# Kernel tuning notes

Measured on AMD Instinct MI355X. Metric: run time of the kernel, lower is better.

Reference implementation:

```python
import jax, jax.numpy as jnp
import numpy as np

B, T, D = 4, 8192, 512
H, BS = 8, 16


def setup_inputs() -> dict:
    key = jax.random.key(0)
    ks = jax.random.split(key, 7)
    s = 1.0 / np.sqrt(D)
    return {
        "x": jax.random.normal(ks[0], (B, T, D), dtype=jnp.float32),
        "Wq": jax.random.normal(ks[1], (D, D), dtype=jnp.float32) * s,
        "bq": jax.random.normal(ks[2], (D,), dtype=jnp.float32) * 0.02,
        "Wk": jax.random.normal(ks[3], (D, D), dtype=jnp.float32) * s,
        "bk": jax.random.normal(ks[4], (D,), dtype=jnp.float32) * 0.02,
        "Wv": jax.random.normal(ks[5], (D, D), dtype=jnp.float32) * s,
        "bv": jax.random.normal(ks[6], (D,), dtype=jnp.float32) * 0.02,
    }


def reference(x, Wq, bq, Wk, bk, Wv, bv):
    b, t, d_model = x.shape
    nb = t // BS          # number of blocks
    dh = d_model // H     # per-head dim
    # [B,T,D] -> [B,nb,BS,D] -> [B,BS,nb,D]: attention runs across blocks
    xb = x.reshape(b, nb, BS, d_model).transpose(0, 2, 1, 3)
    # projections (torch Linear: x @ W.T + b)
    q = xb @ Wq.T + bq
    k = xb @ Wk.T + bk
    v = xb @ Wv.T + bv
    # split heads: [B,BS,nb,H,dh] -> [B,BS,H,nb,dh]
    q = q.reshape(b, BS, nb, H, dh).transpose(0, 1, 3, 2, 4)
    k = k.reshape(b, BS, nb, H, dh).transpose(0, 1, 3, 2, 4)
    v = v.reshape(b, BS, nb, H, dh).transpose(0, 1, 3, 2, 4)
    scale = d_model ** (-0.5)  # note: full dim, as in the original
    attn = jnp.einsum('bshnd,bshmd->bshnm', q, k) * scale  # [B,BS,H,nb,nb]
    attn = jax.nn.softmax(attn, axis=-1)
    out = jnp.einsum('bshnm,bshmd->bshnd', attn, v)        # [B,BS,H,nb,dh]
    # merge heads and undo block permute
    out = out.transpose(0, 1, 3, 2, 4).reshape(b, BS, nb, d_model)
    out = out.transpose(0, 2, 1, 3).reshape(b, t, d_model)
    return out
```

## Files before the change

### kernel.cpp

```cpp
#include <hip/hip_runtime.h>
#include <hip/hip_bf16.h>
#include <cstdint>
#include <cstddef>

#define Bsz 4
#define Tsz 8192
#define Dsz 512
#define Hn 8
#define BSn 16
#define NBn 512
#define DHn 64
#define NQKV 1536
#define MROWS 32768

#define SCL 0.06375870136f
#define ATT_M 8.0f

typedef __attribute__((ext_vector_type(8))) short short8;
typedef __attribute__((ext_vector_type(4))) float float4f;

__device__ __forceinline__ uint16_t f2b(float f) {
  union { float f; uint32_t u; } v; v.f = f;
  uint32_t u = v.u;
  return (uint16_t)((u + 0x7fffu + ((u >> 16) & 1u)) >> 16);
}

__device__ __forceinline__ uint32_t pk2(float a, float b) {
  union { float f; uint32_t u; } x, y; x.f = a; y.f = b;
  return __builtin_amdgcn_perm(y.u + 0x8000u, x.u + 0x8000u, 0x07060302u);
}

__device__ __forceinline__ uint32_t pk2t(float a, float b) {
  union { float f; uint32_t u; } x, y; x.f = a; y.f = b;
  return __builtin_amdgcn_perm(y.u, x.u, 0x07060302u);
}

__device__ __forceinline__ void gl_lds16(const void* g, void* l) {
  __builtin_amdgcn_global_load_lds(
      (const __attribute__((address_space(1))) unsigned int*)g,
      (__attribute__((address_space(3))) unsigned int*)l, 16, 0, 0);
}

#define XBLK (MROWS * Dsz / 1024)
__global__ void cvt_kernel(const float* __restrict__ x, const float* __restrict__ Wq,
                           const float* __restrict__ Wk, const float* __restrict__ Wv,
                           uint16_t* __restrict__ xb, uint16_t* __restrict__ wc) {
  int bid = blockIdx.x;
  if (bid < XBLK) {
    int i = (bid * 256 + threadIdx.x) * 4;
    float4 v = *(const float4*)(x + i);
    uint64_t o = (uint64_t)pk2(v.x, v.y) | ((uint64_t)pk2(v.z, v.w) << 32);
    *(uint64_t*)(xb + i) = o;
  } else {
    int i = ((bid - XBLK) * 256 + threadIdx.x) * 4;
    int row = i >> 9;
    int col = i & 511;
    const float* src = (row < 512) ? Wq : ((row < 1024) ? Wk : Wv);
    float4 v = *(const float4*)(src + (size_t)(row & 511) * 512 + col);
    uint64_t o = (uint64_t)pk2(v.x, v.y) | ((uint64_t)pk2(v.z, v.w) << 32);
    *(uint64_t*)(wc + i) = o;
  }
}

#define BM 128
#define BN 128
#define BK 64

__global__ __launch_bounds__(256, 4) void gemm_qkv(
    const uint16_t* __restrict__ Xb, const uint16_t* __restrict__ Wc,
    const float* __restrict__ bq, const float* __restrict__ bkp,
    const float* __restrict__ bv, uint16_t* __restrict__ Qp,
    uint16_t* __restrict__ Kp, uint16_t* __restrict__ Vtmp) {
  __shared__ uint16_t As[BM * BK];
  __shared__ uint16_t Bs[BN * BK];
  const int tid = threadIdx.x;
  const int wave = tid >> 6, lane = tid & 63;
  const int lrow = lane & 15, quad = lane >> 4;

  int g = blockIdx.x;
  int xcd = g & 7, ii = g >> 3;
  int mt = xcd * 32 + ii / 12;
  int nt = ii - (ii / 12) * 12;
  const int m0 = mt * BM;
  const int n0 = nt * BN;
  const int wm = (wave >> 1) * 64, wn = (wave & 1) * 64;

  float4f acc[4][4] = {};

  for (int k0 = 0; k0 < Dsz; k0 += BK) {
    __syncthreads();
#pragma unroll
    for (int p = 0; p < 4; ++p) {
      int cbase = p * 256 + wave * 64;
      int c = cbase + lane;
      int row = c >> 3, pos = c & 7;
      int kc = (pos ^ (row & 7)) * 8;
      gl_lds16(Xb + (size_t)(m0 + row) * Dsz + k0 + kc, As + cbase * 8);
    }
#pragma unroll
    for (int p = 0; p < 4; ++p) {
      int cbase = p * 256 + wave * 64;
      int c = cbase + lane;
      int row = c >> 3, pos = c & 7;
      int kc = (pos ^ (row & 7)) * 8;
      gl_lds16(Wc + (size_t)(n0 + row) * Dsz + k0 + kc, Bs + cbase * 8);
    }
    __syncthreads();

#pragma unroll
    for (int h = 0; h < 2; ++h) {
      short8 af[4], bf[4];
#pragma unroll
      for (int i = 0; i < 4; ++i) {
        int rowA = wm + i * 16 + lrow;
        af[i] = *(const short8*)(As + rowA * BK + (((h * 4 + quad) ^ (rowA & 7)) * 8));
      }
#pragma unroll
      for (int j = 0; j < 4; ++j) {
        int rowB = wn + j * 16 + lrow;
        bf[j] = *(const short8*)(Bs + rowB * BK + (((h * 4 + quad) ^ (rowB & 7)) * 8));
      }
#pragma unroll
      for (int i = 0; i < 4; ++i)
#pragma unroll
        for (int j = 0; j < 4; ++j)
          acc[i][j] = __builtin_amdgcn_mfma_f32_16x16x32_bf16(af[i], bf[j], acc[i][j], 0, 0, 0);
    }
  }

  const int region = n0 >> 9;
  const float* bias = (region == 0) ? bq : ((region == 1) ? bkp : bv);
  const float mult = (region == 0) ? SCL : 1.0f;
  const int bb = m0 >> 13;
  const int nbbase = ((m0 & 8191) >> 4) + (wm >> 4);
  const int nv0 = (n0 & 511) + wn;

  if (region < 2) {
    uint16_t* dst = (region == 0) ? Qp : Kp;
#pragma unroll
    for (int j = 0; j < 4; ++j) {
      int nl = nv0 + j * 16 + lrow;
      int hh = nl >> 6, dh = nl & 63;
      float bval = bias[nl];
      size_t base = (size_t)bb * 4194304 + (size_t)hh * 32768 +
                    (size_t)nbbase * 64 + dh + (size_t)(quad * 4) * 262144;
#pragma unroll
      for (int i = 0; i < 4; ++i)
#pragma unroll
        for (int r = 0; r < 4; ++r)
          dst[base + (size_t)r * 262144 + (size_t)i * 64] =
              f2b((acc[i][j][r] + bval) * mult);
    }
  } else {
#pragma unroll
    for (int j = 0; j < 4; ++j) {
      int nl = nv0 + j * 16 + lrow;
      float bval = bias[nl];
#pragma unroll
      for (int i = 0; i < 4; ++i) {
        int tok = m0 + wm + i * 16 + quad * 4;
#pragma unroll
        for (int r = 0; r < 4; ++r)
          Vtmp[(size_t)(tok + r) * 512 + nl] = f2b(acc[i][j][r] + bval);
      }
    }
  }
}

__global__ __launch_bounds__(256) void vtrans(const uint16_t* __restrict__ Vtmp,
                                              uint16_t* __restrict__ Vt) {
  __shared__ uint16_t tile[64 * 64];
  int bx = blockIdx.x;
  const int nt = bx & 7; bx >>= 3;
  const int h = bx & 7; bx >>= 3;
  const int s = bx & 15;
  const int b = bx >> 4;
  const int tid = threadIdx.x;

  {
    int i = tid >> 2;
    int token = b * Tsz + (nt * 64 + i) * BSn + s;
    const uint16_t* src = Vtmp + (size_t)token * 512 + h * 64;
#pragma unroll
    for (int hh = 0; hh < 2; ++hh) {
      int ch = (tid & 3) * 2 + hh;
      short8 v = *(const short8*)(src + ch * 8);
      int pc = ch ^ (i & 7);
      *(short8*)(tile + i * 64 + pc * 8) = v;
    }
  }
  __syncthreads();
  {
    int dh = tid & 63, seg = tid >> 6;
    short8 v1, v2;
#pragma unroll
    for (int k = 0; k < 8; ++k) {
      int nb_l = seg * 16 + k;
      v1[k] = (short)tile[nb_l * 64 + (((dh >> 3) ^ (nb_l & 7)) * 8) + (dh & 7)];
    }
#pragma unroll
    for (int k = 0; k < 8; ++k) {
      int nb_l = seg * 16 + 8 + k;
      v2[k] = (short)tile[nb_l * 64 + (((dh >> 3) ^ (nb_l & 7)) * 8) + (dh & 7)];
    }
    size_t obase = ((((size_t)b * 16 + s) * 8 + h) * 64 + dh) * 512 + nt * 64 + seg * 16;
    *(short8*)(Vt + obase) = v1;
    *(short8*)(Vt + obase + 8) = v2;
  }
}

__global__ __launch_bounds__(256, 3) void attn_kernel(
    const uint16_t* __restrict__ Qp, const uint16_t* __restrict__ Kp,
    const uint16_t* __restrict__ Vt, float* __restrict__ out) {
  __shared__ uint16_t Ks[2][32 * 64];
  __shared__ uint16_t Vs[2][64 * 32];
  __shared__ uint16_t Ps[4][4][16 * 32];

  int bx = blockIdx.x;
  const int qh = bx & 1; bx >>= 1;
  const int h = bx & 7; bx >>= 3;
  const int s = bx & 15;
  const int b = bx >> 4;

  const int tid = threadIdx.x;
  const int w = tid >> 6, lane = tid & 63;
  const int lrow = lane & 15, quad = lane >> 4;

  const size_t sh = (((size_t)b * 16 + s) * 8 + h);
  const uint16_t* Qb = Qp + (sh << 15);
  const uint16_t* Kb = Kp + (sh << 15);
  const uint16_t* Vb = Vt + (sh << 15);

  short8 qB[4][2];
  const int q0 = qh * 256 + w * 64;
#pragma unroll
  for (int qs = 0; qs < 4; ++qs) {
    const uint16_t* qp = Qb + (size_t)(q0 + qs * 16 + lrow) * 64;
    qB[qs][0] = *(const short8*)(qp + quad * 8);
    qB[qs][1] = *(const short8*)(qp + 32 + quad * 8);
  }

  float4f O[4][4] = {};
  float l_acc[4] = {0.f, 0.f, 0.f, 0.f};

  const int kr = w * 8 + (lane >> 3);
  const int kcs = (lane & 7) ^ (kr & 7);
  const int vr = w * 16 + (lane >> 2);
  const int vcs = (lane & 3) ^ ((vr >> 1) & 3);

  const int sw = (lrow >> 1) & 3;
  const float4f negm = {-ATT_M, -ATT_M, -ATT_M, -ATT_M};

#define ATT_STAGE(buf, kv0_) do {                                             \
    gl_lds16(Kb + (size_t)((kv0_) + kr) * 64 + kcs * 8, &Ks[buf][w * 512]);   \
    gl_lds16(Vb + (size_t)vr * 512 + (kv0_) + vcs * 8, &Vs[buf][w * 512]);    \
  } while (0)

  ATT_STAGE(0, 0);
  __syncthreads();

  for (int it = 0; it < 16; ++it) {
    const int cur = it & 1;
    if (it < 15) ATT_STAGE(cur ^ 1, (it + 1) * 32);

    {
      short8 kA[2][2];
#pragma unroll
      for (int kt = 0; kt < 2; ++kt) {
        int row = kt * 16 + lrow;
#pragma unroll
        for (int kc = 0; kc < 2; ++kc) {
          int cc = (kc * 4 + quad) ^ (row & 7);
          kA[kt][kc] = *(const short8*)(&Ks[cur][row * 64 + cc * 8]);
        }
      }
#pragma unroll
      for (int qs = 0; qs < 4; ++qs) {
        float4f c0 = negm, c1 = negm;
        __builtin_amdgcn_s_setprio(1);
        c0 = __builtin_amdgcn_mfma_f32_16x16x32_bf16(kA[0][0], qB[qs][0], c0, 0, 0, 0);
        c0 = __builtin_amdgcn_mfma_f32_16x16x32_bf16(kA[0][1], qB[qs][1], c0, 0, 0, 0);
        c1 = __builtin_amdgcn_mfma_f32_16x16x32_bf16(kA[1][0], qB[qs][0], c1, 0, 0, 0);
        c1 = __builtin_amdgcn_mfma_f32_16x16x32_bf16(kA[1][1], qB[qs][1], c1, 0, 0, 0);
        __builtin_amdgcn_s_setprio(0);

        float p00 = __builtin_amdgcn_exp2f(c0[0]);
        float p01 = __builtin_amdgcn_exp2f(c0[1]);
        float p02 = __builtin_amdgcn_exp2f(c0[2]);
        float p03 = __builtin_amdgcn_exp2f(c0[3]);
        float p10 = __builtin_amdgcn_exp2f(c1[0]);
        float p11 = __builtin_amdgcn_exp2f(c1[1]);
        float p12 = __builtin_amdgcn_exp2f(c1[2]);
        float p13 = __builtin_amdgcn_exp2f(c1[3]);
        l_acc[qs] += ((p00 + p01) + (p02 + p03)) + ((p10 + p11) + (p12 + p13));

        uint32_t d0 = pk2t(p00, p01), d1 = pk2t(p02, p03);
        uint32_t d2 = pk2t(p10, p11), d3 = pk2t(p12, p13);
        uint16_t* Psq = Ps[w][qs];
        int half = (quad & 1) * 4;
        *(uint2*)(Psq + lrow * 32 + (((quad >> 1)) ^ sw) * 8 + half) = make_uint2(d0, d1);
        *(uint2*)(Psq + lrow * 32 + ((2 + (quad >> 1)) ^ sw) * 8 + half) = make_uint2(d2, d3);
      }
    }

    {
      short8 vA[4];
#pragma unroll
      for (int dt = 0; dt < 4; ++dt) {
        int row = dt * 16 + lrow;
        vA[dt] = *(const short8*)(&Vs[cur][row * 32 + (quad ^ ((row >> 1) & 3)) * 8]);
      }
#pragma unroll
      for (int qs = 0; qs < 4; ++qs) {
        short8 pB = *(const short8*)(Ps[w][qs] + lrow * 32 + (quad ^ sw) * 8);
        __builtin_amdgcn_s_setprio(1);
#pragma unroll
        for (int dt = 0; dt < 4; ++dt)
          O[dt][qs] = __builtin_amdgcn_mfma_f32_16x16x32_bf16(vA[dt], pB, O[dt][qs], 0, 0, 0);
        __builtin_amdgcn_s_setprio(0);
      }
    }

    if (it < 15) __syncthreads();
  }
#undef ATT_STAGE

#pragma unroll
  for (int qs = 0; qs < 4; ++qs) {
    float l = l_acc[qs];
    l += __shfl_xor(l, 16);
    l += __shfl_xor(l, 32);
    float inv = 1.0f / l;
    int qg = q0 + qs * 16 + lrow;
    float* op = out + ((size_t)b * Tsz + (size_t)qg * 16 + s) * Dsz + h * 64;
#pragma unroll
    for (int dt = 0; dt < 4; ++dt) {
      float4 vv;
      vv.x = O[dt][qs][0] * inv; vv.y = O[dt][qs][1] * inv;
      vv.z = O[dt][qs][2] * inv; vv.w = O[dt][qs][3] * inv;
      *(float4*)(op + dt * 16 + quad * 4) = vv;
    }
  }
}

extern "C" void kernel_launch(void* const* d_in, const int* in_sizes, int n_in,
                              void* d_out, int out_size, void* d_ws, size_t ws_size,
                              hipStream_t stream) {
  const float* x  = (const float*)d_in[0];
  const float* Wq = (const float*)d_in[1];
  const float* bq = (const float*)d_in[2];
  const float* Wk = (const float*)d_in[3];
  const float* bk = (const float*)d_in[4];
  const float* Wv = (const float*)d_in[5];
  const float* bv = (const float*)d_in[6];
  float* out = (float*)d_out;

  uint16_t* Qp   = (uint16_t*)d_ws;
  uint16_t* Kp   = Qp + (size_t)16777216;
  uint16_t* Vtmp = Kp + (size_t)16777216;
  uint16_t* xb   = Vtmp + (size_t)16777216;
  uint16_t* wc   = xb + (size_t)16777216;
  uint16_t* Vt   = xb;

  hipLaunchKernelGGL(cvt_kernel, dim3(XBLK + NQKV * Dsz / 1024), dim3(256), 0, stream,
                     x, Wq, Wk, Wv, xb, wc);
  hipLaunchKernelGGL(gemm_qkv, dim3((MROWS / BM) * (NQKV / BN)), dim3(256), 0, stream,
                     xb, wc, bq, bk, bv, Qp, Kp, Vtmp);
  hipLaunchKernelGGL(vtrans, dim3(Bsz * BSn * Hn * 8), dim3(256), 0, stream, Vtmp, Vt);
  hipLaunchKernelGGL(attn_kernel, dim3(Bsz * BSn * Hn * 2), dim3(256), 0, stream,
                     Qp, Kp, Vt, out);
}
```

Baseline: 261.1 us.

## Drop V transpose kernel; read V row-major and transpose via ds_read_b64_tr_b16

Removes the separate vtrans kernel that wrote a transposed copy of V to global memory. The attention kernel now stages V tiles straight from the projection output (token-major layout) into LDS and uses the gfx950 LDS transpose-read instruction to build the MFMA A operands. This saves one kernel launch and a full read+write pass over V. In exchange it adds inline asm with a full lgkmcnt wait and a strided global gather per stage.

```diff
diff --git a/kernel.cpp b/kernel.cpp
--- a/kernel.cpp
+++ b/kernel.cpp
@@ -17,6 +17,7 @@
 #define ATT_M 8.0f
 
 typedef __attribute__((ext_vector_type(8))) short short8;
+typedef __attribute__((ext_vector_type(4))) short short4v;
 typedef __attribute__((ext_vector_type(4))) float float4f;
 
 __device__ __forceinline__ uint16_t f2b(float f) {
@@ -167,53 +168,11 @@
   }
 }
 
-__global__ __launch_bounds__(256) void vtrans(const uint16_t* __restrict__ Vtmp,
-                                              uint16_t* __restrict__ Vt) {
-  __shared__ uint16_t tile[64 * 64];
-  int bx = blockIdx.x;
-  const int nt = bx & 7; bx >>= 3;
-  const int h = bx & 7; bx >>= 3;
-  const int s = bx & 15;
-  const int b = bx >> 4;
-  const int tid = threadIdx.x;
-
-  {
-    int i = tid >> 2;
-    int token = b * Tsz + (nt * 64 + i) * BSn + s;
-    const uint16_t* src = Vtmp + (size_t)token * 512 + h * 64;
-#pragma unroll
-    for (int hh = 0; hh < 2; ++hh) {
-      int ch = (tid & 3) * 2 + hh;
-      short8 v = *(const short8*)(src + ch * 8);
-      int pc = ch ^ (i & 7);
-      *(short8*)(tile + i * 64 + pc * 8) = v;
-    }
-  }
-  __syncthreads();
-  {
-    int dh = tid & 63, seg = tid >> 6;
-    short8 v1, v2;
-#pragma unroll
-    for (int k = 0; k < 8; ++k) {
-      int nb_l = seg * 16 + k;
-      v1[k] = (short)tile[nb_l * 64 + (((dh >> 3) ^ (nb_l & 7)) * 8) + (dh & 7)];
-    }
-#pragma unroll
-    for (int k = 0; k < 8; ++k) {
-      int nb_l = seg * 16 + 8 + k;
-      v2[k] = (short)tile[nb_l * 64 + (((dh >> 3) ^ (nb_l & 7)) * 8) + (dh & 7)];
-    }
-    size_t obase = ((((size_t)b * 16 + s) * 8 + h) * 64 + dh) * 512 + nt * 64 + seg * 16;
-    *(short8*)(Vt + obase) = v1;
-    *(short8*)(Vt + obase + 8) = v2;
-  }
-}
-
 __global__ __launch_bounds__(256, 3) void attn_kernel(
     const uint16_t* __restrict__ Qp, const uint16_t* __restrict__ Kp,
-    const uint16_t* __restrict__ Vt, float* __restrict__ out) {
+    const uint16_t* __restrict__ Vtmp, float* __restrict__ out) {
   __shared__ uint16_t Ks[2][32 * 64];
-  __shared__ uint16_t Vs[2][64 * 32];
+  __shared__ uint16_t Vs[2][32 * 64];
   __shared__ uint16_t Ps[4][4][16 * 32];
 
   int bx = blockIdx.x;
@@ -229,7 +188,14 @@
   const size_t sh = (((size_t)b * 16 + s) * 8 + h);
   const uint16_t* Qb = Qp + (sh << 15);
   const uint16_t* Kb = Kp + (sh << 15);
-  const uint16_t* Vb = Vt + (sh << 15);
+
+  const int e_hi = tid >> 7, dtv = (tid >> 5) & 3, qv = (tid >> 3) & 3,
+            jv = (tid >> 1) & 3, hbv = tid & 1;
+  const int kvv = qv * 8 + e_hi * 4 + jv;
+  const uint16_t* vsrc = Vtmp + ((size_t)b * Tsz + s) * 512 +
+                         (size_t)kvv * 8192 + h * 64 + dtv * 16 + hbv * 8;
+  const unsigned vs_base =
+      (unsigned)(uintptr_t)(__attribute__((address_space(3))) const uint16_t*)&Vs[0][0];
 
   short8 qB[4][2];
   const int q0 = qh * 256 + w * 64;
@@ -245,15 +211,13 @@
 
   const int kr = w * 8 + (lane >> 3);
   const int kcs = (lane & 7) ^ (kr & 7);
-  const int vr = w * 16 + (lane >> 2);
-  const int vcs = (lane & 3) ^ ((vr >> 1) & 3);
 
   const int sw = (lrow >> 1) & 3;
   const float4f negm = {-ATT_M, -ATT_M, -ATT_M, -ATT_M};
 
 #define ATT_STAGE(buf, kv0_) do {                                             \
     gl_lds16(Kb + (size_t)((kv0_) + kr) * 64 + kcs * 8, &Ks[buf][w * 512]);   \
-    gl_lds16(Vb + (size_t)vr * 512 + (kv0_) + vcs * 8, &Vs[buf][w * 512]);    \
+    gl_lds16(vsrc + (size_t)(kv0_) * 8192, &Vs[buf][w * 512]);                \
   } while (0)
 
   ATT_STAGE(0, 0);
@@ -304,12 +268,27 @@
     }
 
     {
+      short4v t0, t1, t2, t3, t4, t5, t6, t7;
+      unsigned vaddr = vs_base + (cur << 12) + (lane << 3);
+      asm volatile(
+          "ds_read_b64_tr_b16 %0, %8\n\t"
+          "ds_read_b64_tr_b16 %1, %8 offset:2048\n\t"
+          "ds_read_b64_tr_b16 %2, %8 offset:512\n\t"
+          "ds_read_b64_tr_b16 %3, %8 offset:2560\n\t"
+          "ds_read_b64_tr_b16 %4, %8 offset:1024\n\t"
+          "ds_read_b64_tr_b16 %5, %8 offset:3072\n\t"
+          "ds_read_b64_tr_b16 %6, %8 offset:1536\n\t"
+          "ds_read_b64_tr_b16 %7, %8 offset:3584\n\t"
+          "s_waitcnt lgkmcnt(0)"
+          : "=&v"(t0), "=&v"(t1), "=&v"(t2), "=&v"(t3),
+            "=&v"(t4), "=&v"(t5), "=&v"(t6), "=&v"(t7)
+          : "v"(vaddr));
+      __builtin_amdgcn_sched_barrier(0);
       short8 vA[4];
-#pragma unroll
-      for (int dt = 0; dt < 4; ++dt) {
-        int row = dt * 16 + lrow;
-        vA[dt] = *(const short8*)(&Vs[cur][row * 32 + (quad ^ ((row >> 1) & 3)) * 8]);
-      }
+      vA[0] = __builtin_shufflevector(t0, t1, 0, 1, 2, 3, 4, 5, 6, 7);
+      vA[1] = __builtin_shufflevector(t2, t3, 0, 1, 2, 3, 4, 5, 6, 7);
+      vA[2] = __builtin_shufflevector(t4, t5, 0, 1, 2, 3, 4, 5, 6, 7);
+      vA[3] = __builtin_shufflevector(t6, t7, 0, 1, 2, 3, 4, 5, 6, 7);
 #pragma unroll
       for (int qs = 0; qs < 4; ++qs) {
         short8 pB = *(const short8*)(Ps[w][qs] + lrow * 32 + (quad ^ sw) * 8);
@@ -360,13 +339,11 @@
   uint16_t* Vtmp = Kp + (size_t)16777216;
   uint16_t* xb   = Vtmp + (size_t)16777216;
   uint16_t* wc   = xb + (size_t)16777216;
-  uint16_t* Vt   = xb;
 
   hipLaunchKernelGGL(cvt_kernel, dim3(XBLK + NQKV * Dsz / 1024), dim3(256), 0, stream,
                      x, Wq, Wk, Wv, xb, wc);
   hipLaunchKernelGGL(gemm_qkv, dim3((MROWS / BM) * (NQKV / BN)), dim3(256), 0, stream,
                      xb, wc, bq, bk, bv, Qp, Kp, Vtmp);
-  hipLaunchKernelGGL(vtrans, dim3(Bsz * BSn * Hn * 8), dim3(256), 0, stream, Vtmp, Vt);
   hipLaunchKernelGGL(attn_kernel, dim3(Bsz * BSn * Hn * 2), dim3(256), 0, stream,
-                     Qp, Kp, Vt, out);
-}
+                     Qp, Kp, Vtmp, out);
+}
```

After: 239.1 us, median of 3. 8.4% less time.
